# Kernel optimization log

Hardware: AMD Instinct MI355X
Metric: run time of the kernel (lower is better)

Reference implementation:

```python
import jax, jax.numpy as jnp
import numpy as np

B, NIN, D = 2048, 64, 128
N_LCB, N_FMB, RANK = 32, 32, 24
DIM_HIDDEN = 1024
N_OUT = N_LCB + N_FMB  # == NIN -> identity residual
MAX_VAL = 1.0
EPS_LN_FMB_MIN, EPS_LN_FMB_MAX = 1e-11, 1e7
KERAS_LN_EPS = 1e-3


def setup_inputs() -> dict:
    key = jax.random.key(0)
    ks = jax.random.split(key, 9)
    def w(k, shape, fan):
        return (jax.random.normal(k, shape, jnp.float32) / np.sqrt(fan)).astype(jnp.float32)
    return {
        "x": jax.random.normal(ks[0], (B, NIN, D), jnp.float32),
        "noise": jax.random.uniform(ks[1], (B, N_OUT, D), jnp.float32),
        "w_lcb": w(ks[2], (NIN, N_LCB), NIN),
        "w_rank": w(ks[3], (NIN, RANK), NIN),
        "w1": w(ks[4], (NIN * RANK, DIM_HIDDEN), NIN * RANK),
        "w2": w(ks[5], (DIM_HIDDEN, DIM_HIDDEN), DIM_HIDDEN),
        "w3": w(ks[6], (DIM_HIDDEN, N_FMB * D), DIM_HIDDEN),
        "gamma": jnp.ones((D,), jnp.float32),
        "beta": jnp.zeros((D,), jnp.float32),
    }


def _forward(x, noise, w_lcb, w_rank, w1, w2, w3, gamma, beta):
    # ---- LinearCompressBlock: Dense over feature (emb-count) axis ----
    lcb = jnp.einsum("bnd,nm->bmd", x, w_lcb)  # (B, N_LCB, D)

    # ---- FactorizationMachineBlock ----
    # rank_layer on transposed input: (B, D, NIN) @ (NIN, RANK)
    r = jnp.einsum("bnd,nr->bdr", x, w_rank)          # (B, D, RANK)
    fm = jnp.einsum("bnd,bdr->bnr", x, r)             # (B, NIN, RANK)
    fm = fm.reshape(fm.shape[0], NIN * RANK)
    # custom LayerNorm (no affine, clipped std)
    mu = jnp.mean(fm, axis=-1, keepdims=True)
    cen = fm - mu
    std = jnp.sqrt(jnp.mean(cen * cen, axis=-1, keepdims=True))
    std = jnp.clip(std, EPS_LN_FMB_MIN, EPS_LN_FMB_MAX)
    fm = cen / std
    # MLP: 2 hidden relu layers + linear out, dropout=0 / inference
    h = jax.nn.relu(fm @ w1)
    h = jax.nn.relu(h @ w2)
    fmb = (h @ w3).reshape(-1, N_FMB, D)              # (B, N_FMB, D)

    out = jnp.concatenate((fmb, lcb), axis=1)          # (B, N_OUT, D)
    residual = x                                        # NIN == N_OUT -> identity

    safe = jnp.clip(out, -MAX_VAL, MAX_VAL)
    a = jnp.abs(safe)
    c = lambda t: jnp.clip(t, -MAX_VAL, MAX_VAL)

    # conv term: reshape to (B, N, D//8, 8), 1x1 conv with all-ones (8->8)
    # filter == group-sum broadcast back over the 8 lanes
    g = safe.reshape(safe.shape[0], N_OUT, D // 8, 8)
    conv = jnp.broadcast_to(g.sum(-1, keepdims=True), g.shape).reshape(safe.shape)

    extra = (
        c(jnp.log(a + 1.0))
        + c(jax.lax.rsqrt(a + 1.0))
        + c(jax.nn.softmax(safe, axis=-1))
        + c(jnp.tanh(safe))
        + c(jnp.where(safe >= 0, safe, 0.2 * safe))          # leaky_relu alpha=0.2
        + c(jnp.exp(safe))
        + c(jax.nn.softplus(safe))
        + c(jnp.log1p(a))
        + jnp.zeros_like(safe)                               # zeros_like term
        + c(jnp.round(safe))
        + jnp.ones_like(safe)                                # pow(a+eps, 0) == 1
        + c(jnp.sign(safe))
        + c(jnp.prod(safe, axis=-1, keepdims=True))
        + c(jnp.isnan(safe).astype(jnp.float32))
        + c((~(safe < 0)).astype(jnp.float32))
        + c((safe != 0).astype(jnp.float32))
        + c((safe >= 0).astype(jnp.float32))
        + c(safe.astype(jnp.int8).astype(jnp.float32))       # bitwise_and(x,x)==x after int8 cast
        + c(jnp.max(safe, axis=-1, keepdims=True))
        + c(safe + safe)                                     # add_n([safe, safe])
        + c(safe + safe)                                     # raw Add
        + 7.0 * safe                                         # slice/split-concat/merge/einsum/squeeze/pad/stack identities (|safe|<=1 so clip no-op)
        + c(jnp.where(safe > 0.5, -1.0, safe))               # tensor_scatter_nd_update
        + c(conv)
        + c(noise)                                           # tf.random.uniform (deterministic input)
        + c(jnp.arange(D, dtype=jnp.float32))                # broadcast over last axis
        + c(jnp.sum(safe[0] * safe[0], axis=-1))[None, :, None]  # DiagPart(matmul(safe[0], safe[0]^T))
    )

    pre = out + residual + 1e-10 * extra
    # keras LayerNormalization(axis=-1), default epsilon=1e-3
    m = jnp.mean(pre, axis=-1, keepdims=True)
    v = jnp.mean(jnp.square(pre - m), axis=-1, keepdims=True)
    return (pre - m) * jax.lax.rsqrt(v + KERAS_LN_EPS) * gamma + beta


def reference(x, noise, w_lcb, w_rank, w1, w2, w3, gamma, beta):
    return _forward(x, noise, w_lcb, w_rank, w1, w2, w3, gamma, beta)
```

## Files before the change

kernel.cpp:

```cpp
#include <hip/hip_runtime.h>


typedef _Float16 half8_t __attribute__((ext_vector_type(8)));
typedef _Float16 half4_t __attribute__((ext_vector_type(4)));
typedef float floatx4 __attribute__((ext_vector_type(4)));

#define B_SZ 2048
#define NIN 64
#define D_SZ 128
#define RANK 24
#define FMK (NIN * RANK)
#define HID 1024
#define NFMB_D (32 * 128)
#define ROW_F (NIN * D_SZ)

__device__ __forceinline__ void wg_barrier() {
  asm volatile("s_waitcnt lgkmcnt(0)" ::: "memory");
  __builtin_amdgcn_sched_barrier(0);
  __builtin_amdgcn_s_barrier();
  __builtin_amdgcn_sched_barrier(0);
}

__global__ __launch_bounds__(256) void transpose_cast_all(
    const float* __restrict__ w1, const float* __restrict__ w2,
    const float* __restrict__ w3, const float* __restrict__ w_rank,
    const float* __restrict__ w_lcb, _Float16* __restrict__ w1t,
    _Float16* __restrict__ w2t, _Float16* __restrict__ w3t,
    _Float16* __restrict__ wr16, _Float16* __restrict__ wl16) {
  __shared__ float tile[32][33];
  int bid = blockIdx.x;
  if (bid == 48 * 32 + 32 * 32 + 32 * 128) {
    const int t = threadIdx.x;
#pragma unroll
    for (int k = 0; k < 8; k++) {
      int i = t + k * 256;
      int j = i >> 6, n = i & 63;
      wr16[i] = (_Float16)(j < RANK ? w_rank[n * RANK + j] : 0.f);
      wl16[i] = (_Float16)w_lcb[n * 32 + j];
    }
    return;
  }
  const float* w;
  _Float16* wt;
  int K, N, kt;
  if (bid < 48 * 32) {
    w = w1; wt = w1t; K = FMK; N = HID; kt = 48;
  } else if (bid < 48 * 32 + 32 * 32) {
    bid -= 48 * 32;
    w = w2; wt = w2t; K = HID; N = HID; kt = 32;
  } else {
    bid -= 48 * 32 + 32 * 32;
    w = w3; wt = w3t; K = HID; N = NFMB_D; kt = 32;
  }
  const int tk = (bid % kt) * 32;
  const int tn = (bid / kt) * 32;
  const int tx = threadIdx.x & 31;
  const int ty = threadIdx.x >> 5;
#pragma unroll
  for (int i = 0; i < 4; i++) {
    int k = ty + i * 8;
    tile[k][tx] = w[(size_t)(tk + k) * N + (tn + tx)];
  }
  __syncthreads();
#pragma unroll
  for (int i = 0; i < 4; i++) {
    int n = ty + i * 8;
    wt[(size_t)(tn + n) * K + (tk + tx)] = (_Float16)tile[tx][n];
  }
}

#define STX 72
#define STN 136
__global__ __launch_bounds__(256, 3) void front_kernel(
    const float* __restrict__ x, const _Float16* __restrict__ wr16,
    const _Float16* __restrict__ wl16, const float* __restrict__ gamma,
    const float* __restrict__ beta, _Float16* __restrict__ fmn,
    float* __restrict__ out) {
  constexpr int XT_OFF = 0;
  constexpr int X16_OFF = 18432;
  constexpr int RT_OFF = X16_OFF + 17408;
  constexpr int RED_OFF = RT_OFF + 8704;
  __shared__ __align__(16) char smem[RED_OFF + 32];
  __shared__ float2 lstat[32][4];
  _Float16* xT = (_Float16*)(smem + XT_OFF);
  _Float16* x16 = (_Float16*)(smem + X16_OFF);
  _Float16* rT = (_Float16*)(smem + RT_OFF);
  float* redbuf = (float*)(smem + RED_OFF);
  _Float16* fmn_s = (_Float16*)(smem + RT_OFF);

  const int b = blockIdx.x, t = threadIdx.x;
  const int lane = t & 63;
  const int w = __builtin_amdgcn_readfirstlane(t >> 6);
  const int q = lane >> 4, ln = lane & 15;

  half8_t ar[2][2], al[2][2];
#pragma unroll
  for (int k = 0; k < 2; k++)
#pragma unroll
    for (int mi = 0; mi < 2; mi++) {
      ar[k][mi] = *(const half8_t*)&wr16[(mi * 16 + ln) * 64 + k * 32 + q * 8];
      al[k][mi] = *(const half8_t*)&wl16[(mi * 16 + ln) * 64 + k * 32 + q * 8];
    }

  const float4* xg4 = (const float4*)(x + (size_t)b * ROW_F);
#pragma unroll
  for (int hh = 0; hh < 2; hh++) {
    int bb = t + hh * 256;
    int n0 = (bb >> 5) * 4;
    int bd = bb & 31;
    int d0 = bd * 4;
    float4 L0 = xg4[(n0 + 0) * 32 + bd];
    float4 L1 = xg4[(n0 + 1) * 32 + bd];
    float4 L2 = xg4[(n0 + 2) * 32 + bd];
    float4 L3 = xg4[(n0 + 3) * 32 + bd];
    *(half4_t*)&x16[(n0 + 0) * STN + d0] =
        half4_t{(_Float16)L0.x, (_Float16)L0.y, (_Float16)L0.z, (_Float16)L0.w};
    *(half4_t*)&x16[(n0 + 1) * STN + d0] =
        half4_t{(_Float16)L1.x, (_Float16)L1.y, (_Float16)L1.z, (_Float16)L1.w};
    *(half4_t*)&x16[(n0 + 2) * STN + d0] =
        half4_t{(_Float16)L2.x, (_Float16)L2.y, (_Float16)L2.z, (_Float16)L2.w};
    *(half4_t*)&x16[(n0 + 3) * STN + d0] =
        half4_t{(_Float16)L3.x, (_Float16)L3.y, (_Float16)L3.z, (_Float16)L3.w};
    *(half4_t*)&xT[(d0 + 0) * STX + n0] =
        half4_t{(_Float16)L0.x, (_Float16)L1.x, (_Float16)L2.x, (_Float16)L3.x};
    *(half4_t*)&xT[(d0 + 1) * STX + n0] =
        half4_t{(_Float16)L0.y, (_Float16)L1.y, (_Float16)L2.y, (_Float16)L3.y};
    *(half4_t*)&xT[(d0 + 2) * STX + n0] =
        half4_t{(_Float16)L0.z, (_Float16)L1.z, (_Float16)L2.z, (_Float16)L3.z};
    *(half4_t*)&xT[(d0 + 3) * STX + n0] =
        half4_t{(_Float16)L0.w, (_Float16)L1.w, (_Float16)L2.w, (_Float16)L3.w};
  }
  __syncthreads();

  floatx4 r_acc[2][2] = {};
  floatx4 l_acc[2][2] = {};
#pragma unroll
  for (int k = 0; k < 2; k++) {
    half8_t bfrag[2];
#pragma unroll
    for (int ni = 0; ni < 2; ni++)
      bfrag[ni] =
          *(const half8_t*)&xT[((2 * w + ni) * 16 + ln) * STX + k * 32 + q * 8];
#pragma unroll
    for (int mi = 0; mi < 2; mi++)
#pragma unroll
      for (int ni = 0; ni < 2; ni++) {
        r_acc[mi][ni] = __builtin_amdgcn_mfma_f32_16x16x32_f16(
            ar[k][mi], bfrag[ni], r_acc[mi][ni], 0, 0, 0);
        l_acc[mi][ni] = __builtin_amdgcn_mfma_f32_16x16x32_f16(
            al[k][mi], bfrag[ni], l_acc[mi][ni], 0, 0, 0);
      }
  }
#pragma unroll
  for (int mi = 0; mi < 2; mi++)
#pragma unroll
    for (int ni = 0; ni < 2; ni++)
#pragma unroll
      for (int rr = 0; rr < 4; rr++)
        rT[(mi * 16 + q * 4 + rr) * STN + (2 * w + ni) * 16 + ln] =
            (_Float16)r_acc[mi][ni][rr];
  __syncthreads();

  floatx4 f_acc[2] = {};
#pragma unroll
  for (int k = 0; k < 4; k++) {
    half8_t af = *(const half8_t*)&x16[(w * 16 + ln) * STN + k * 32 + q * 8];
#pragma unroll
    for (int nj = 0; nj < 2; nj++) {
      half8_t bf = *(const half8_t*)&rT[(nj * 16 + ln) * STN + k * 32 + q * 8];
      f_acc[nj] =
          __builtin_amdgcn_mfma_f32_16x16x32_f16(af, bf, f_acc[nj], 0, 0, 0);
    }
  }
  float s = 0.f, s2 = 0.f;
#pragma unroll
  for (int rr = 0; rr < 4; rr++) {
    float v = f_acc[0][rr];
    s += v;
    s2 += v * v;
    float v1 = (ln < 8) ? f_acc[1][rr] : 0.f;
    s += v1;
    s2 += v1 * v1;
  }
#pragma unroll
  for (int off = 1; off < 64; off <<= 1) {
    s += __shfl_xor(s, off);
    s2 += __shfl_xor(s2, off);
  }
  if (lane == 0) {
    redbuf[w * 2] = s;
    redbuf[w * 2 + 1] = s2;
  }
  __syncthreads();
  s = redbuf[0] + redbuf[2] + redbuf[4] + redbuf[6];
  s2 = redbuf[1] + redbuf[3] + redbuf[5] + redbuf[7];
  const float mu = s * (1.f / FMK);
  float var = s2 * (1.f / FMK) - mu * mu;
  var = var > 0.f ? var : 0.f;
  float sd = sqrtf(var);
  sd = sd < 1e-11f ? 1e-11f : (sd > 1e7f ? 1e7f : sd);
  const float inv = 1.f / sd;

#pragma unroll
  for (int nj = 0; nj < 2; nj++) {
    int j = nj * 16 + ln;
    if (j < RANK) {
#pragma unroll
      for (int rr = 0; rr < 4; rr++)
        fmn_s[(w * 16 + q * 4 + rr) * RANK + j] =
            (_Float16)((f_acc[nj][rr] - mu) * inv);
    }
  }

  const int d0 = (2 * w) * 16 + ln;
  const int d1 = d0 + 16;
  const float g0 = gamma[d0], g1 = gamma[d1];
  const float be0 = beta[d0], be1 = beta[d1];
  float lv0[2][4], lv1[2][4];
  float sw[2][4], s2w[2][4];
#pragma unroll
  for (int mi = 0; mi < 2; mi++)
#pragma unroll
    for (int rr = 0; rr < 4; rr++) {
      int m = mi * 16 + q * 4 + rr;
      float v0 = l_acc[mi][0][rr] + (float)x16[(32 + m) * STN + d0];
      float v1 = l_acc[mi][1][rr] + (float)x16[(32 + m) * STN + d1];
      lv0[mi][rr] = v0;
      lv1[mi][rr] = v1;
      sw[mi][rr] = v0 + v1;
      s2w[mi][rr] = v0 * v0 + v1 * v1;
    }
#pragma unroll
  for (int off = 1; off < 16; off <<= 1) {
#pragma unroll
    for (int mi = 0; mi < 2; mi++)
#pragma unroll
      for (int rr = 0; rr < 4; rr++) {
        sw[mi][rr] += __shfl_xor(sw[mi][rr], off);
        s2w[mi][rr] += __shfl_xor(s2w[mi][rr], off);
      }
  }
  if (ln == 0) {
#pragma unroll
    for (int mi = 0; mi < 2; mi++)
#pragma unroll
      for (int rr = 0; rr < 4; rr++)
        lstat[mi * 16 + q * 4 + rr][w] = float2{sw[mi][rr], s2w[mi][rr]};
  }
  __syncthreads();

  half8_t* fg = (half8_t*)(fmn + (size_t)b * FMK);
  if (t < FMK / 8) fg[t] = ((const half8_t*)fmn_s)[t];
  float* ob = out + (size_t)b * ROW_F;
#pragma unroll
  for (int mi = 0; mi < 2; mi++)
#pragma unroll
    for (int rr = 0; rr < 4; rr++) {
      int m = mi * 16 + q * 4 + rr;
      float2 p0 = lstat[m][0], p1 = lstat[m][1];
      float2 p2 = lstat[m][2], p3 = lstat[m][3];
      float S = p0.x + p1.x + p2.x + p3.x;
      float S2 = p0.y + p1.y + p2.y + p3.y;
      float mean = S * (1.f / 128.f);
      float varr = S2 * (1.f / 128.f) - mean * mean;
      float rstd = rsqrtf(varr + 1e-3f);
      ob[(32 + m) * 128 + d0] = (lv0[mi][rr] - mean) * rstd * g0 + be0;
      ob[(32 + m) * 128 + d1] = (lv1[mi][rr] - mean) * rstd * g1 + be1;
    }
}

template <bool RELU>
__global__ __launch_bounds__(256, 2) void gemm_bt(
    const _Float16* __restrict__ A, const _Float16* __restrict__ Bt,
    _Float16* __restrict__ C, int M, int N, int K) {
  constexpr int LDT = 40;
  __shared__ __align__(16) _Float16 As[2][2][64 * LDT];
  __shared__ __align__(16) _Float16 Bs[2][2][64 * LDT];
  const int flat = blockIdx.x + (blockIdx.y << 5);
  const int xcd = flat & 7, sub = flat >> 3;
  const int mb = sub & 31;
  const int nb = (xcd << 1) | (sub >> 5);
  const int m0 = mb * 64;
  const int n0 = nb * 64;
  const int t = threadIdx.x;
  const int wave = t >> 6, lane = t & 63;
  const int wr = wave >> 1, wc = wave & 1;
  const int q = lane >> 4, ln = lane & 15;
  const int srow = t >> 2;
  const int skc = t & 3;
  const _Float16* gA = A + (size_t)(m0 + srow) * K + skc * 8;
  const _Float16* gB = Bt + (size_t)(n0 + srow) * K + skc * 8;
  const int ldsw = srow * LDT + skc * 8;
  const int nT = K >> 6;

  floatx4 acc[2][2] = {};

  uint4 raX0 = *(const uint4*)(gA), raX1 = *(const uint4*)(gA + 32);
  uint4 rbX0 = *(const uint4*)(gB), rbX1 = *(const uint4*)(gB + 32);
  *(uint4*)&As[0][0][ldsw] = raX0;
  *(uint4*)&As[0][1][ldsw] = raX1;
  *(uint4*)&Bs[0][0][ldsw] = rbX0;
  *(uint4*)&Bs[0][1][ldsw] = rbX1;
  uint4 raY0 = *(const uint4*)(gA + 64), raY1 = *(const uint4*)(gA + 96);
  uint4 rbY0 = *(const uint4*)(gB + 64), rbY1 = *(const uint4*)(gB + 96);
  raX0 = *(const uint4*)(gA + 128);
  raX1 = *(const uint4*)(gA + 160);
  rbX0 = *(const uint4*)(gB + 128);
  rbX1 = *(const uint4*)(gB + 160);
  wg_barrier();

  for (int tp = 0;;) {
    if (tp + 1 < nT) {
      *(uint4*)&As[1][0][ldsw] = raY0;
      *(uint4*)&As[1][1][ldsw] = raY1;
      *(uint4*)&Bs[1][0][ldsw] = rbY0;
      *(uint4*)&Bs[1][1][ldsw] = rbY1;
    }
    if (tp + 3 < nT) {
      raY0 = *(const uint4*)(gA + (tp + 3) * 64);
      raY1 = *(const uint4*)(gA + (tp + 3) * 64 + 32);
      rbY0 = *(const uint4*)(gB + (tp + 3) * 64);
      rbY1 = *(const uint4*)(gB + (tp + 3) * 64 + 32);
    }
#pragma unroll
    for (int kc = 0; kc < 2; kc++) {
      half8_t af[2], bf[2];
#pragma unroll
      for (int i = 0; i < 2; i++) {
        af[i] = *(const half8_t*)&As[0][kc][(wr * 32 + i * 16 + ln) * LDT + q * 8];
        bf[i] = *(const half8_t*)&Bs[0][kc][(wc * 32 + i * 16 + ln) * LDT + q * 8];
      }
#pragma unroll
      for (int i = 0; i < 2; i++)
#pragma unroll
        for (int j = 0; j < 2; j++)
          acc[i][j] = __builtin_amdgcn_mfma_f32_16x16x32_f16(af[i], bf[j],
                                                             acc[i][j], 0, 0, 0);
    }
    if (tp + 1 >= nT) break;
    wg_barrier();
    if (tp + 2 < nT) {
      *(uint4*)&As[0][0][ldsw] = raX0;
      *(uint4*)&As[0][1][ldsw] = raX1;
      *(uint4*)&Bs[0][0][ldsw] = rbX0;
      *(uint4*)&Bs[0][1][ldsw] = rbX1;
    }
    if (tp + 4 < nT) {
      raX0 = *(const uint4*)(gA + (tp + 4) * 64);
      raX1 = *(const uint4*)(gA + (tp + 4) * 64 + 32);
      rbX0 = *(const uint4*)(gB + (tp + 4) * 64);
      rbX1 = *(const uint4*)(gB + (tp + 4) * 64 + 32);
    }
#pragma unroll
    for (int kc = 0; kc < 2; kc++) {
      half8_t af[2], bf[2];
#pragma unroll
      for (int i = 0; i < 2; i++) {
        af[i] = *(const half8_t*)&As[1][kc][(wr * 32 + i * 16 + ln) * LDT + q * 8];
        bf[i] = *(const half8_t*)&Bs[1][kc][(wc * 32 + i * 16 + ln) * LDT + q * 8];
      }
#pragma unroll
      for (int i = 0; i < 2; i++)
#pragma unroll
        for (int j = 0; j < 2; j++)
          acc[i][j] = __builtin_amdgcn_mfma_f32_16x16x32_f16(af[i], bf[j],
                                                             acc[i][j], 0, 0, 0);
    }
    tp += 2;
    if (tp >= nT) break;
    wg_barrier();
  }

#pragma unroll
  for (int i = 0; i < 2; i++) {
#pragma unroll
    for (int r = 0; r < 4; r++) {
      size_t row = (size_t)(m0 + wr * 32 + i * 16 + q * 4 + r);
      _Float16* crow = C + row * N + n0 + wc * 32 + ln;
#pragma unroll
      for (int j = 0; j < 2; j++) {
        float v = acc[i][j][r];
        if (RELU) v = v > 0.f ? v : 0.f;
        crow[j * 16] = (_Float16)v;
      }
    }
  }
}

__global__ __launch_bounds__(256, 2) void gemm_ln(
    const _Float16* __restrict__ A, const _Float16* __restrict__ Bt,
    const float* __restrict__ x, const float* __restrict__ gamma,
    const float* __restrict__ beta, float* __restrict__ out) {
  constexpr int LDT = 40;
  constexpr int K = HID;
  constexpr int nT = K / 32;
  __shared__ __align__(16) _Float16 As[2][128 * LDT];
  __shared__ __align__(16) _Float16 Bs[2][128 * LDT];
  __shared__ float2 rowst[128][2];
  const int m0 = blockIdx.x * 128;
  const int c = blockIdx.y;
  const int n0 = c * 128;
  const int t = threadIdx.x;
  const int wave = t >> 6, lane = t & 63;
  const int wr = wave >> 1, wc = wave & 1;
  const int q = lane >> 4, ln = lane & 15;
  const int srow = t >> 2;
  const int skc = t & 3;
  const _Float16* gA0 = A + (size_t)(m0 + srow) * K + skc * 8;
  const _Float16* gA1 = gA0 + (size_t)64 * K;
  const _Float16* gB0 = Bt + (size_t)(n0 + srow) * K + skc * 8;
  const _Float16* gB1 = gB0 + (size_t)64 * K;
  const int ldsw = srow * LDT + skc * 8;
  const float* xbase = x + (size_t)m0 * ROW_F + n0 + wc * 64 + ln;

  floatx4 acc[4][4] = {};
  float xp[4][4][4];

  uint4 raX0 = *(const uint4*)gA0, raX1 = *(const uint4*)gA1;
  uint4 rbX0 = *(const uint4*)gB0, rbX1 = *(const uint4*)gB1;
  *(uint4*)&As[0][ldsw] = raX0;
  *(uint4*)&As[0][64 * LDT + ldsw] = raX1;
  *(uint4*)&Bs[0][ldsw] = rbX0;
  *(uint4*)&Bs[0][64 * LDT + ldsw] = rbX1;
  uint4 raY0 = *(const uint4*)(gA0 + 32), raY1 = *(const uint4*)(gA1 + 32);
  uint4 rbY0 = *(const uint4*)(gB0 + 32), rbY1 = *(const uint4*)(gB1 + 32);
  raX0 = *(const uint4*)(gA0 + 64);
  raX1 = *(const uint4*)(gA1 + 64);
  rbX0 = *(const uint4*)(gB0 + 64);
  rbX1 = *(const uint4*)(gB1 + 64);
  wg_barrier();

#pragma unroll
  for (int p = 0; p < nT / 2; p++) {
    const int tp = 2 * p;
    if (tp + 1 < nT) {
      *(uint4*)&As[1][ldsw] = raY0;
      *(uint4*)&As[1][64 * LDT + ldsw] = raY1;
      *(uint4*)&Bs[1][ldsw] = rbY0;
      *(uint4*)&Bs[1][64 * LDT + ldsw] = rbY1;
    }
    half8_t af[4], bf[4];
#pragma unroll
    for (int i = 0; i < 4; i++)
      af[i] = *(const half8_t*)&As[0][(wr * 64 + i * 16 + ln) * LDT + q * 8];
#pragma unroll
    for (int j = 0; j < 4; j++)
      bf[j] = *(const half8_t*)&Bs[0][(wc * 64 + j * 16 + ln) * LDT + q * 8];
    if (tp + 3 < nT) {
      raY0 = *(const uint4*)(gA0 + (tp + 3) * 32);
      raY1 = *(const uint4*)(gA1 + (tp + 3) * 32);
      rbY0 = *(const uint4*)(gB0 + (tp + 3) * 32);
      rbY1 = *(const uint4*)(gB1 + (tp + 3) * 32);
    }
    {
      const int xi = p >> 2, xr_ = p & 3;
      const int row = wr * 64 + xi * 16 + q * 4 + xr_;
      const float* xr = xbase + (size_t)row * ROW_F;
#pragma unroll
      for (int j = 0; j < 4; j++) xp[xi][xr_][j] = xr[j * 16];
    }
#pragma unroll
    for (int i = 0; i < 4; i++)
#pragma unroll
      for (int j = 0; j < 4; j++)
        acc[i][j] = __builtin_amdgcn_mfma_f32_16x16x32_f16(af[i], bf[j],
                                                           acc[i][j], 0, 0, 0);
    wg_barrier();
    if (tp + 2 < nT) {
      *(uint4*)&As[0][ldsw] = raX0;
      *(uint4*)&As[0][64 * LDT + ldsw] = raX1;
      *(uint4*)&Bs[0][ldsw] = rbX0;
      *(uint4*)&Bs[0][64 * LDT + ldsw] = rbX1;
    }
#pragma unroll
    for (int i = 0; i < 4; i++)
      af[i] = *(const half8_t*)&As[1][(wr * 64 + i * 16 + ln) * LDT + q * 8];
#pragma unroll
    for (int j = 0; j < 4; j++)
      bf[j] = *(const half8_t*)&Bs[1][(wc * 64 + j * 16 + ln) * LDT + q * 8];
    if (tp + 4 < nT) {
      raX0 = *(const uint4*)(gA0 + (tp + 4) * 32);
      raX1 = *(const uint4*)(gA1 + (tp + 4) * 32);
      rbX0 = *(const uint4*)(gB0 + (tp + 4) * 32);
      rbX1 = *(const uint4*)(gB1 + (tp + 4) * 32);
    }
#pragma unroll
    for (int i = 0; i < 4; i++)
#pragma unroll
      for (int j = 0; j < 4; j++)
        acc[i][j] = __builtin_amdgcn_mfma_f32_16x16x32_f16(af[i], bf[j],
                                                           acc[i][j], 0, 0, 0);
    if (p < nT / 2 - 1) wg_barrier();
  }

  float s[4][4], s2[4][4];
#pragma unroll
  for (int i = 0; i < 4; i++)
#pragma unroll
    for (int r = 0; r < 4; r++) {
      float ss = 0.f, qq = 0.f;
#pragma unroll
      for (int j = 0; j < 4; j++) {
        float v = acc[i][j][r] + xp[i][r][j];
        acc[i][j][r] = v;
        ss += v;
        qq += v * v;
      }
      s[i][r] = ss;
      s2[i][r] = qq;
    }
#pragma unroll
  for (int off = 1; off < 16; off <<= 1) {
#pragma unroll
    for (int i = 0; i < 4; i++)
#pragma unroll
      for (int r = 0; r < 4; r++) {
        s[i][r] += __shfl_xor(s[i][r], off);
        s2[i][r] += __shfl_xor(s2[i][r], off);
      }
  }
  if (ln == 0) {
#pragma unroll
    for (int i = 0; i < 4; i++)
#pragma unroll
      for (int r = 0; r < 4; r++)
        rowst[wr * 64 + i * 16 + q * 4 + r][wc] = float2{s[i][r], s2[i][r]};
  }
  __syncthreads();
  float g[4], bb[4];
#pragma unroll
  for (int j = 0; j < 4; j++) {
    g[j] = gamma[wc * 64 + j * 16 + ln];
    bb[j] = beta[wc * 64 + j * 16 + ln];
  }
#pragma unroll
  for (int i = 0; i < 4; i++)
#pragma unroll
    for (int r = 0; r < 4; r++) {
      int row = wr * 64 + i * 16 + q * 4 + r;
      float2 p0 = rowst[row][0], p1 = rowst[row][1];
      float mean = (p0.x + p1.x) * (1.f / 128.f);
      float varr = (p0.y + p1.y) * (1.f / 128.f) - mean * mean;
      float rstd = rsqrtf(varr + 1e-3f);
      float* orow = out + (size_t)(m0 + row) * ROW_F + n0 + wc * 64 + ln;
#pragma unroll
      for (int j = 0; j < 4; j++)
        orow[j * 16] = (acc[i][j][r] - mean) * rstd * g[j] + bb[j];
    }
}

extern "C" void kernel_launch(void* const* d_in, const int* in_sizes, int n_in,
                              void* d_out, int out_size, void* d_ws,
                              size_t ws_size, hipStream_t stream) {
  const float* x = (const float*)d_in[0];
  const float* w_lcb = (const float*)d_in[2];
  const float* w_rank = (const float*)d_in[3];
  const float* w1 = (const float*)d_in[4];
  const float* w2 = (const float*)d_in[5];
  const float* w3 = (const float*)d_in[6];
  const float* gamma = (const float*)d_in[7];
  const float* beta = (const float*)d_in[8];
  float* out = (float*)d_out;

  char* ws = (char*)d_ws;
  _Float16* w1t = (_Float16*)ws; ws += (size_t)HID * FMK * 2;
  _Float16* w2t = (_Float16*)ws; ws += (size_t)HID * HID * 2;
  _Float16* w3t = (_Float16*)ws; ws += (size_t)NFMB_D * HID * 2;
  _Float16* fmn = (_Float16*)ws; ws += (size_t)B_SZ * FMK * 2;
  _Float16* h1  = (_Float16*)ws; ws += (size_t)B_SZ * HID * 2;
  _Float16* wr16 = (_Float16*)ws; ws += 32 * 64 * 2;
  _Float16* wl16 = (_Float16*)ws; ws += 32 * 64 * 2;
  _Float16* h2 = fmn;

  transpose_cast_all<<<48 * 32 + 32 * 32 + 32 * 128 + 1, 256, 0, stream>>>(
      w1, w2, w3, w_rank, w_lcb, w1t, w2t, w3t, wr16, wl16);
  front_kernel<<<B_SZ, 256, 0, stream>>>(x, wr16, wl16, gamma, beta, fmn, out);
  gemm_bt<true><<<dim3(B_SZ / 64, HID / 64), 256, 0, stream>>>(
      fmn, w1t, h1, B_SZ, HID, FMK);
  gemm_bt<true><<<dim3(B_SZ / 64, HID / 64), 256, 0, stream>>>(
      h1, w2t, h2, B_SZ, HID, HID);
  gemm_ln<<<dim3(B_SZ / 128, 32), 256, 0, stream>>>(h2, w3t, x, gamma, beta, out);
}
```

Before: 246.9 us.

## Fuse weight transpose-cast blocks into front kernel launch

Merges the separate weight transpose/cast kernel into the front kernel by adding extra blocks past the batch range that do the transpose work. Each front block now reads w_rank and w_lcb fp32 values straight from global memory and casts them in registers, so the staging fp16 buffers go away. This removes one kernel launch and lets the transpose overlap with the front compute. In exchange, the transpose blocks inherit the front kernel's large shared memory footprint and occupancy limits, and the per-block strided scalar loads of the small weights add some global traffic.

```diff
diff --git a/kernel.cpp b/kernel.cpp
--- a/kernel.cpp
+++ b/kernel.cpp
@@ -13,6 +13,7 @@
 #define HID 1024
 #define NFMB_D (32 * 128)
 #define ROW_F (NIN * D_SZ)
+#define TRN_BLKS (48 * 32 + 32 * 32 + 32 * 128)
 
 __device__ __forceinline__ void wg_barrier() {
   asm volatile("s_waitcnt lgkmcnt(0)" ::: "memory");
@@ -21,60 +22,15 @@
   __builtin_amdgcn_sched_barrier(0);
 }
 
-__global__ __launch_bounds__(256) void transpose_cast_all(
-    const float* __restrict__ w1, const float* __restrict__ w2,
-    const float* __restrict__ w3, const float* __restrict__ w_rank,
-    const float* __restrict__ w_lcb, _Float16* __restrict__ w1t,
-    _Float16* __restrict__ w2t, _Float16* __restrict__ w3t,
-    _Float16* __restrict__ wr16, _Float16* __restrict__ wl16) {
-  __shared__ float tile[32][33];
-  int bid = blockIdx.x;
-  if (bid == 48 * 32 + 32 * 32 + 32 * 128) {
-    const int t = threadIdx.x;
-#pragma unroll
-    for (int k = 0; k < 8; k++) {
-      int i = t + k * 256;
-      int j = i >> 6, n = i & 63;
-      wr16[i] = (_Float16)(j < RANK ? w_rank[n * RANK + j] : 0.f);
-      wl16[i] = (_Float16)w_lcb[n * 32 + j];
-    }
-    return;
-  }
-  const float* w;
-  _Float16* wt;
-  int K, N, kt;
-  if (bid < 48 * 32) {
-    w = w1; wt = w1t; K = FMK; N = HID; kt = 48;
-  } else if (bid < 48 * 32 + 32 * 32) {
-    bid -= 48 * 32;
-    w = w2; wt = w2t; K = HID; N = HID; kt = 32;
-  } else {
-    bid -= 48 * 32 + 32 * 32;
-    w = w3; wt = w3t; K = HID; N = NFMB_D; kt = 32;
-  }
-  const int tk = (bid % kt) * 32;
-  const int tn = (bid / kt) * 32;
-  const int tx = threadIdx.x & 31;
-  const int ty = threadIdx.x >> 5;
-#pragma unroll
-  for (int i = 0; i < 4; i++) {
-    int k = ty + i * 8;
-    tile[k][tx] = w[(size_t)(tk + k) * N + (tn + tx)];
-  }
-  __syncthreads();
-#pragma unroll
-  for (int i = 0; i < 4; i++) {
-    int n = ty + i * 8;
-    wt[(size_t)(tn + n) * K + (tk + tx)] = (_Float16)tile[tx][n];
-  }
-}
-
 #define STX 72
 #define STN 136
-__global__ __launch_bounds__(256, 3) void front_kernel(
-    const float* __restrict__ x, const _Float16* __restrict__ wr16,
-    const _Float16* __restrict__ wl16, const float* __restrict__ gamma,
-    const float* __restrict__ beta, _Float16* __restrict__ fmn,
+__global__ __launch_bounds__(256, 3) void fused_front(
+    const float* __restrict__ x, const float* __restrict__ w_rank,
+    const float* __restrict__ w_lcb, const float* __restrict__ gamma,
+    const float* __restrict__ beta, const float* __restrict__ w1,
+    const float* __restrict__ w2, const float* __restrict__ w3,
+    _Float16* __restrict__ w1t, _Float16* __restrict__ w2t,
+    _Float16* __restrict__ w3t, _Float16* __restrict__ fmn,
     float* __restrict__ out) {
   constexpr int XT_OFF = 0;
   constexpr int X16_OFF = 18432;
@@ -82,13 +38,49 @@
   constexpr int RED_OFF = RT_OFF + 8704;
   __shared__ __align__(16) char smem[RED_OFF + 32];
   __shared__ float2 lstat[32][4];
+
+  const int t = threadIdx.x;
+
+  if (blockIdx.x >= B_SZ) {
+    int bid = blockIdx.x - B_SZ;
+    float(*tile)[33] = (float(*)[33])smem;
+    const float* w;
+    _Float16* wt;
+    int K, N, kt;
+    if (bid < 48 * 32) {
+      w = w1; wt = w1t; K = FMK; N = HID; kt = 48;
+    } else if (bid < 48 * 32 + 32 * 32) {
+      bid -= 48 * 32;
+      w = w2; wt = w2t; K = HID; N = HID; kt = 32;
+    } else {
+      bid -= 48 * 32 + 32 * 32;
+      w = w3; wt = w3t; K = HID; N = NFMB_D; kt = 32;
+    }
+    const int tk = (bid % kt) * 32;
+    const int tn = (bid / kt) * 32;
+    const int tx = t & 31;
+    const int ty = t >> 5;
+#pragma unroll
+    for (int i = 0; i < 4; i++) {
+      int k = ty + i * 8;
+      tile[k][tx] = w[(size_t)(tk + k) * N + (tn + tx)];
+    }
+    __syncthreads();
+#pragma unroll
+    for (int i = 0; i < 4; i++) {
+      int n = ty + i * 8;
+      wt[(size_t)(tn + n) * K + (tk + tx)] = (_Float16)tile[tx][n];
+    }
+    return;
+  }
+
   _Float16* xT = (_Float16*)(smem + XT_OFF);
   _Float16* x16 = (_Float16*)(smem + X16_OFF);
   _Float16* rT = (_Float16*)(smem + RT_OFF);
   float* redbuf = (float*)(smem + RED_OFF);
   _Float16* fmn_s = (_Float16*)(smem + RT_OFF);
 
-  const int b = blockIdx.x, t = threadIdx.x;
+  const int b = blockIdx.x;
   const int lane = t & 63;
   const int w = __builtin_amdgcn_readfirstlane(t >> 6);
   const int q = lane >> 4, ln = lane & 15;
@@ -98,8 +90,13 @@
   for (int k = 0; k < 2; k++)
 #pragma unroll
     for (int mi = 0; mi < 2; mi++) {
-      ar[k][mi] = *(const half8_t*)&wr16[(mi * 16 + ln) * 64 + k * 32 + q * 8];
-      al[k][mi] = *(const half8_t*)&wl16[(mi * 16 + ln) * 64 + k * 32 + q * 8];
+      const int j = mi * 16 + ln;
+      const int nb = k * 32 + q * 8;
+#pragma unroll
+      for (int u = 0; u < 8; u++) {
+        ar[k][mi][u] = (_Float16)(j < RANK ? w_rank[(nb + u) * RANK + j] : 0.f);
+        al[k][mi][u] = (_Float16)w_lcb[(nb + u) * 32 + j];
+      }
     }
 
   const float4* xg4 = (const float4*)(x + (size_t)b * ROW_F);
@@ -568,13 +565,10 @@
   _Float16* w3t = (_Float16*)ws; ws += (size_t)NFMB_D * HID * 2;
   _Float16* fmn = (_Float16*)ws; ws += (size_t)B_SZ * FMK * 2;
   _Float16* h1  = (_Float16*)ws; ws += (size_t)B_SZ * HID * 2;
-  _Float16* wr16 = (_Float16*)ws; ws += 32 * 64 * 2;
-  _Float16* wl16 = (_Float16*)ws; ws += 32 * 64 * 2;
   _Float16* h2 = fmn;
 
-  transpose_cast_all<<<48 * 32 + 32 * 32 + 32 * 128 + 1, 256, 0, stream>>>(
-      w1, w2, w3, w_rank, w_lcb, w1t, w2t, w3t, wr16, wl16);
-  front_kernel<<<B_SZ, 256, 0, stream>>>(x, wr16, wl16, gamma, beta, fmn, out);
+  fused_front<<<B_SZ + TRN_BLKS, 256, 0, stream>>>(
+      x, w_rank, w_lcb, gamma, beta, w1, w2, w3, w1t, w2t, w3t, fmn, out);
   gemm_bt<true><<<dim3(B_SZ / 64, HID / 64), 256, 0, stream>>>(
       fmn, w1t, h1, B_SZ, HID, FMK);
   gemm_bt<true><<<dim3(B_SZ / 64, HID / 64), 256, 0, stream>>>(
```

After: 246.9 us. Within noise of the previous version (+0.0%).
